# Kernel tuning notes

Hardware: AMD Instinct MI355X
Metric: run time of the kernel (lower is better)

The kernel has to match this reference:

```python
import jax, jax.numpy as jnp
import numpy as np

H = 16  # n_heads (init kwarg)


def pos_enc(length, dim):
    # torch PositionalEncoding: pe[:,0::2]=sin, pe[:,1::2]=cos
    pos = jnp.arange(length, dtype=jnp.float32)[:, None]
    div = jnp.exp(jnp.arange(0, dim, 2, dtype=jnp.float32) * (-np.log(10000.0) / dim))
    ang = pos * div  # [L, dim/2]
    return jnp.stack([jnp.sin(ang), jnp.cos(ang)], axis=-1).reshape(length, dim)


def torch_ln(x, a, b, eps=1e-6):
    # custom LayerNorm: a*(x-mean)/(std+eps)+b with unbiased std (torch default)
    mean = x.mean(-1, keepdims=True)
    n = x.shape[-1]
    var = ((x - mean) ** 2).sum(-1, keepdims=True) / (n - 1)
    return a * (x - mean) / (jnp.sqrt(var) + eps) + b


def setup_inputs() -> dict:
    key = jax.random.key(0)
    ks = jax.random.split(key, 16)
    B, Lq, Lk, qd, kd, hid, mid = 8, 512, 1024, 768, 768, 1024, 4096
    s = 0.02  # weight init scale
    w = lambda k, shape: jax.random.normal(k, shape, jnp.float32) * s
    return dict(
        q=jax.random.normal(ks[0], (B, Lq, qd), jnp.float32),
        k=jax.random.normal(ks[1], (B, Lk, kd), jnp.float32),
        Wq=w(ks[2], (qd, hid)), bq=jnp.zeros(hid, jnp.float32),
        Wk=w(ks[3], (kd, hid)), bk=jnp.zeros(hid, jnp.float32),
        Wv=w(ks[4], (kd, hid)), bv=jnp.zeros(hid, jnp.float32),
        Wv0=w(ks[5], (kd, hid)), bv0=jnp.zeros(hid, jnp.float32),
        Wq0=w(ks[6], (qd, hid)), bq0=jnp.zeros(hid, jnp.float32),
        nq_a=jnp.ones(hid, jnp.float32), nq_b=jnp.zeros(hid, jnp.float32),
        nx_a=jnp.ones(hid, jnp.float32), nx_b=jnp.zeros(hid, jnp.float32),
        W1=w(ks[7], (hid, mid)), b1=jnp.zeros(mid, jnp.float32),
        W2=w(ks[8], (mid, hid)), b2=jnp.zeros(hid, jnp.float32),
        ns_a=jnp.ones(hid, jnp.float32), ns_b=jnp.zeros(hid, jnp.float32),
    )


def reference(q, k, Wq, bq, Wk, bk, Wv, bv, Wv0, bv0, Wq0, bq0,
              nq_a, nq_b, nx_a, nx_b, W1, b1, W2, b2, ns_a, ns_b):
    # FocalAtt(mode='CA').forward(q, k, PE='qk', SF=True, outmode='atted_bilinear')
    B, Lq, qd = q.shape
    Lk, kd = k.shape[1], k.shape[2]
    hid = Wq.shape[1]
    dh = hid // H
    q0 = q
    qp = q + pos_enc(Lq, qd)  # PosEnc_q (dropout=0)
    kp = k + pos_enc(Lk, kd)  # PosEnc_k
    # AttM: manual multi-head scores
    qh = (qp @ Wq + bq).reshape(B, Lq, H, dh).transpose(0, 2, 1, 3)  # bhqd
    kh = (kp @ Wk + bk).reshape(B, Lk, H, dh).transpose(0, 2, 1, 3)  # bhkd
    scores = jnp.einsum('bhqd,bhkd->bhqk', qh, kh) / jnp.sqrt(jnp.float32(dh))
    att = jax.nn.softmax(scores, axis=-1)  # SF=True
    q0p = q0 @ Wq0 + bq0  # [B, Lq, hid]
    # 'atted' branch
    v1 = (kp @ Wv + bv).reshape(B, Lk, H, dh).transpose(0, 2, 1, 3)
    atted = jnp.einsum('bhqk,bhkd->bhqd', att, v1)
    atted = atted.transpose(0, 2, 1, 3).reshape(B, Lq, hid)
    atted = torch_ln(q0p + atted, nq_a, nq_b)
    # 'bilinear' branch: einsum('bhvk,bhvq,bhqk->bhk')
    q0h = q0p.reshape(B, Lq, H, dh).transpose(0, 2, 1, 3)  # bhvd, v=Lq
    v0 = (kp @ Wv0 + bv0).reshape(B, Lk, H, dh).transpose(0, 2, 1, 3)  # bhqd, q=Lk
    x = jnp.einsum('bhvd,bhvq,bhqd->bhd', q0h, att, v0).reshape(B, hid)
    x = torch_ln(x, nx_a, nx_b)
    # attention output: relu over scores, mean over heads
    att_out = jax.nn.relu(scores).sum(axis=1) / jnp.float32(H)  # [B, Lq, Lk]
    # SorCA: FFN + residual + LayerNorm
    ff = jax.nn.relu(atted @ W1 + b1) @ W2 + b2
    qq = torch_ln(atted + ff, ns_a, ns_b)
    # FocalAtt returns (feature, q, k, attention, attidx_q, attidx_k); drop Nones
    return (x, qq, kp, att_out)
```

## Files before the change

### kernel.cpp

```cpp
#include <hip/hip_runtime.h>


typedef unsigned short bfr;
using short8 = __attribute__((ext_vector_type(8))) short;
using f32x4  = __attribute__((ext_vector_type(4))) float;

__device__ __forceinline__ float b2f(bfr s) {
  return __uint_as_float(((unsigned int)s) << 16);
}
__device__ __forceinline__ bfr f2b(float f) {
  unsigned int u = __float_as_uint(f);
  u += 0x7fffu + ((u >> 16) & 1u);
  return (bfr)(u >> 16);
}

struct __align__(8) us4 { bfr x, y, z, w; };

__device__ __forceinline__ float4 load4f(const float* p) { return *(const float4*)p; }
__device__ __forceinline__ float4 load4f(const bfr* p) {
  us4 u = *(const us4*)p;
  return make_float4(b2f(u.x), b2f(u.y), b2f(u.z), b2f(u.w));
}
__device__ __forceinline__ void store4(float* p, float a, float b, float c, float d) {
  *(float4*)p = make_float4(a, b, c, d);
}
__device__ __forceinline__ void store4(bfr* p, float a, float b, float c, float d) {
  us4 v; v.x = f2b(a); v.y = f2b(b); v.z = f2b(c); v.w = f2b(d);
  *(us4*)p = v;
}

__device__ __forceinline__ void gll16(const bfr* g, bfr* l) {
  __builtin_amdgcn_global_load_lds(
      (const __attribute__((address_space(1))) unsigned int*)g,
      (__attribute__((address_space(3))) unsigned int*)l, 16, 0, 0);
}

__device__ __forceinline__ float pe_val(int l, int d) {
  float ang = (float)l * expf((float)(d & ~1) * (-9.210340371976184f / 768.0f));
  return (d & 1) ? cosf(ang) : sinf(ang);
}

__global__ __launch_bounds__(256) void posenc_k(const float* __restrict__ in,
                                                float* __restrict__ outf,
                                                bfr* __restrict__ outb, int total) {
  int idx = blockIdx.x * 256 + threadIdx.x;
  if (idx >= total) return;
  float v = in[idx] + pe_val((idx / 768) % 1024, idx % 768);
  outf[idx] = v;
  outb[idx] = f2b(v);
}

__global__ __launch_bounds__(256) void posenc_q_all(const float* __restrict__ in,
                                                    bfr* __restrict__ out,
                                                    bfr* __restrict__ outraw,
                                                    int total) {
  int idx = blockIdx.x * 256 + threadIdx.x;
  if (idx >= total) return;
  float v = in[idx];
  out[idx] = f2b(v + pe_val((idx / 768) % 512, idx % 768));
  outraw[idx] = f2b(v);
}

__global__ __launch_bounds__(256) void transpose_w(const float* __restrict__ src,
                                                   bfr* __restrict__ dst,
                                                   int rows, int cols, int ld,
                                                   int mode) {
  __shared__ float t[32][33];
  const int bc = blockIdx.x * 32, br = blockIdx.y * 32;
  const int tx = threadIdx.x & 31, ty = threadIdx.x >> 5;
#pragma unroll
  for (int i = 0; i < 4; i++)
    t[ty + i * 8][tx] = src[(size_t)(br + ty + i * 8) * ld + bc + tx];
  __syncthreads();
#pragma unroll
  for (int i = 0; i < 4; i++) {
    int c = bc + ty + i * 8;
    int r = (mode == 0) ? c : ((c >> 6) * 128 + (c & 63) + (mode == 2 ? 64 : 0));
    dst[(size_t)r * rows + br + tx] = f2b(t[tx][ty + i * 8]);
  }
}

template <typename TC>
__device__ __forceinline__ void mgemm_body(const bfr* __restrict__ A,
                                           const bfr* __restrict__ BT,
                                           const float* __restrict__ bias,
                                           TC* __restrict__ C,
                                           int K, int ldc, int relu, int accum,
                                           int m0, int n0,
                                           bfr* __restrict__ As,
                                           bfr* __restrict__ Bs) {
  const int tid = threadIdx.x;
  const int lane = tid & 63, w = tid >> 6;
  const int wm = (w & 1) * 64, wn = (w >> 1) * 64;
  const int grow = w * 32 + (lane >> 3);
  const int gkc = (lane & 7) * 8;
  const int fr = lane & 15, fc = (lane >> 4) * 8;
  const int NT = K >> 6;
  f32x4 acc[4][4];
#pragma unroll
  for (int i = 0; i < 4; i++)
#pragma unroll
    for (int j = 0; j < 4; j++) acc[i][j] = (f32x4){0.f, 0.f, 0.f, 0.f};

  auto issue = [&](int t, int buf) {
    const int k0 = t << 6;
    const bfr* Ag = A + (size_t)(m0 + grow) * K + k0 + gkc;
    const bfr* Bg = BT + (size_t)(n0 + grow) * K + k0 + gkc;
#pragma unroll
    for (int i = 0; i < 4; i++)
      gll16(Ag + (size_t)(i * 8) * K, As + buf * 8192 + (w * 32 + i * 8) * 64);
#pragma unroll
    for (int i = 0; i < 4; i++)
      gll16(Bg + (size_t)(i * 8) * K, Bs + buf * 8192 + (w * 32 + i * 8) * 64);
  };

  issue(0, 0);
  __syncthreads();
  int cur = 0;
  for (int t = 0; t < NT; ++t) {
    const bool more = (t + 1 < NT);
    if (more) issue(t + 1, cur ^ 1);
    __builtin_amdgcn_s_setprio(1);
#pragma unroll
    for (int ks = 0; ks < 2; ks++) {
      short8 af[4], bf4[4];
#pragma unroll
      for (int i = 0; i < 4; i++)
        af[i] = *(const short8*)(As + cur * 8192 + (wm + i * 16 + fr) * 64 + ks * 32 + fc);
#pragma unroll
      for (int i = 0; i < 4; i++)
        bf4[i] = *(const short8*)(Bs + cur * 8192 + (wn + i * 16 + fr) * 64 + ks * 32 + fc);
#pragma unroll
      for (int i = 0; i < 4; i++)
#pragma unroll
        for (int j = 0; j < 4; j++)
          acc[i][j] = __builtin_amdgcn_mfma_f32_16x16x32_bf16(af[i], bf4[j], acc[i][j], 0, 0, 0);
    }
    __builtin_amdgcn_s_setprio(0);
    if (more) {
      __syncthreads();
      cur ^= 1;
    }
  }
  const int col0 = n0 + wn + fr;
  const int row0 = m0 + wm + (lane >> 4) * 4;
  float bsv[4];
#pragma unroll
  for (int j = 0; j < 4; j++) bsv[j] = bias ? bias[col0 + j * 16] : 0.f;
#pragma unroll
  for (int i = 0; i < 4; i++) {
#pragma unroll
    for (int j = 0; j < 4; j++) {
      const int col = col0 + j * 16;
#pragma unroll
      for (int r = 0; r < 4; r++) {
        const int row = row0 + i * 16 + r;
        float v = acc[i][j][r] + bsv[j];
        if (relu) v = fmaxf(v, 0.f);
        size_t idx = (size_t)row * ldc + col;
        if constexpr (sizeof(TC) == 2) {
          C[idx] = f2b(v);
        } else {
          if (accum) C[idx] += v; else C[idx] = v;
        }
      }
    }
  }
}

template <typename TC>
__device__ __forceinline__ void mgemm_body64(const bfr* __restrict__ A,
                                             const bfr* __restrict__ BT,
                                             const float* __restrict__ bias,
                                             TC* __restrict__ C,
                                             int K, int ldc, int relu, int accum,
                                             int m0, int n0,
                                             bfr* __restrict__ As,
                                             bfr* __restrict__ Bs) {
  const int tid = threadIdx.x;
  const int lane = tid & 63, w = tid >> 6;
  const int wm = (w & 1) * 64, wn = (w >> 1) * 32;
  const int grow = lane >> 3, gkc = (lane & 7) * 8;
  const int fr = lane & 15, fc = (lane >> 4) * 8;
  const int NT = K >> 6;
  f32x4 acc[4][2];
#pragma unroll
  for (int i = 0; i < 4; i++)
#pragma unroll
    for (int j = 0; j < 2; j++) acc[i][j] = (f32x4){0.f, 0.f, 0.f, 0.f};

  auto issue = [&](int t, int buf) {
    const int k0 = t << 6;
    const bfr* Ag = A + (size_t)(m0 + w * 32 + grow) * K + k0 + gkc;
#pragma unroll
    for (int i = 0; i < 4; i++)
      gll16(Ag + (size_t)(i * 8) * K, As + buf * 8192 + (w * 32 + i * 8) * 64);
    const bfr* Bg = BT + (size_t)(n0 + w * 16 + grow) * K + k0 + gkc;
#pragma unroll
    for (int i = 0; i < 2; i++)
      gll16(Bg + (size_t)(i * 8) * K, Bs + buf * 4096 + (w * 16 + i * 8) * 64);
  };

  issue(0, 0);
  __syncthreads();
  int cur = 0;
  for (int t = 0; t < NT; ++t) {
    const bool more = (t + 1 < NT);
    if (more) issue(t + 1, cur ^ 1);
    __builtin_amdgcn_s_setprio(1);
#pragma unroll
    for (int ks = 0; ks < 2; ks++) {
      short8 af[4], bf4[2];
#pragma unroll
      for (int i = 0; i < 4; i++)
        af[i] = *(const short8*)(As + cur * 8192 + (wm + i * 16 + fr) * 64 + ks * 32 + fc);
#pragma unroll
      for (int j = 0; j < 2; j++)
        bf4[j] = *(const short8*)(Bs + cur * 4096 + (wn + j * 16 + fr) * 64 + ks * 32 + fc);
#pragma unroll
      for (int i = 0; i < 4; i++)
#pragma unroll
        for (int j = 0; j < 2; j++)
          acc[i][j] = __builtin_amdgcn_mfma_f32_16x16x32_bf16(af[i], bf4[j], acc[i][j], 0, 0, 0);
    }
    __builtin_amdgcn_s_setprio(0);
    if (more) {
      __syncthreads();
      cur ^= 1;
    }
  }
  const int col0 = n0 + wn + fr;
  const int row0 = m0 + wm + (lane >> 4) * 4;
  float bsv[2];
#pragma unroll
  for (int j = 0; j < 2; j++) bsv[j] = bias ? bias[col0 + j * 16] : 0.f;
#pragma unroll
  for (int i = 0; i < 4; i++) {
#pragma unroll
    for (int j = 0; j < 2; j++) {
      const int col = col0 + j * 16;
#pragma unroll
      for (int r = 0; r < 4; r++) {
        const int row = row0 + i * 16 + r;
        float v = acc[i][j][r] + bsv[j];
        if (relu) v = fmaxf(v, 0.f);
        size_t idx = (size_t)row * ldc + col;
        if constexpr (sizeof(TC) == 2) {
          C[idx] = f2b(v);
        } else {
          if (accum) C[idx] += v; else C[idx] = v;
        }
      }
    }
  }
}

template <typename TC>
__global__ __launch_bounds__(256) void mgemm(const bfr* __restrict__ A,
                                             const bfr* __restrict__ BT,
                                             const float* __restrict__ bias,
                                             TC* __restrict__ C,
                                             int K, int ldc, int relu, int accum) {
  __shared__ bfr As[2][8192];
  __shared__ bfr Bs[2][8192];
  const int nwg = gridDim.x * gridDim.y;
  const int bid = blockIdx.y * gridDim.x + blockIdx.x;
  const int q8 = nwg >> 3, r8 = nwg & 7;
  const int xcd = bid & 7, off = bid >> 3;
  const int swz = (xcd < r8 ? xcd * (q8 + 1) : r8 * (q8 + 1) + (xcd - r8) * q8) + off;
  const int n0 = (swz % gridDim.x) * 128, m0 = (swz / gridDim.x) * 128;
  mgemm_body<TC>(A, BT, bias, C, K, ldc, relu, accum, m0, n0,
                 &As[0][0], &Bs[0][0]);
}

template <typename TC>
__global__ __launch_bounds__(256) void mgemm64(const bfr* __restrict__ A,
                                               const bfr* __restrict__ BT,
                                               const float* __restrict__ bias,
                                               TC* __restrict__ C,
                                               int K, int ldc, int relu, int accum) {
  __shared__ bfr As[2][8192];
  __shared__ bfr Bs[2][4096];
  const int nwg = gridDim.x * gridDim.y;
  const int bid = blockIdx.y * gridDim.x + blockIdx.x;
  const int q8 = nwg >> 3, r8 = nwg & 7;
  const int xcd = bid & 7, off = bid >> 3;
  const int swz = (xcd < r8 ? xcd * (q8 + 1) : r8 * (q8 + 1) + (xcd - r8) * q8) + off;
  const int n0 = (swz % gridDim.x) * 64, m0 = (swz / gridDim.x) * 128;
  mgemm_body64<TC>(A, BT, bias, C, K, ldc, relu, accum, m0, n0,
                   &As[0][0], &Bs[0][0]);
}

__global__ __launch_bounds__(256) void kv_gemm2(const bfr* __restrict__ kp0,
                                                const bfr* __restrict__ kp1,
                                                const bfr* __restrict__ WkT,
                                                const float* __restrict__ bk,
                                                bfr* __restrict__ kh0,
                                                bfr* __restrict__ kh1,
                                                const bfr* __restrict__ WTvv,
                                                bfr* __restrict__ vT0,
                                                bfr* __restrict__ vT1) {
  __shared__ bfr As[2][8192];
  __shared__ bfr Bs[2][4096];
  const int swz = (blockIdx.x & 7) * 96 + (blockIdx.x >> 3);
  if (swz < 128) {
    mgemm_body64<bfr>(kp0, WkT, bk, kh0, 768, 1024, 0, 0,
                      (swz >> 4) * 128, (swz & 15) * 64, &As[0][0], &Bs[0][0]);
  } else if (swz < 256) {
    const int s = swz - 128;
    mgemm_body64<bfr>(kp1, WkT, bk, kh1, 768, 1024, 0, 0,
                      (s >> 4) * 128, (s & 15) * 64, &As[0][0], &Bs[0][0]);
  } else if (swz < 512) {
    const int s = swz - 256;
    mgemm_body64<bfr>(WTvv, kp0, nullptr, vT0, 768, 1024, 0, 0,
                      (s >> 4) * 128, (s & 15) * 64, &As[0][0], &Bs[0][0]);
  } else {
    const int s = swz - 512;
    mgemm_body64<bfr>(WTvv, kp1, nullptr, vT1, 768, 1024, 0, 0,
                      (s >> 4) * 128, (s & 15) * 64, &As[0][0], &Bs[0][0]);
  }
}

__global__ __launch_bounds__(256) void proj_gemm(const bfr* __restrict__ q16,
                                                 const bfr* __restrict__ Wq0T,
                                                 const float* __restrict__ bq0,
                                                 bfr* __restrict__ q0p,
                                                 const bfr* __restrict__ qp_all,
                                                 const bfr* __restrict__ WqT,
                                                 const float* __restrict__ bq,
                                                 bfr* __restrict__ qh) {
  __shared__ bfr As[2][8192];
  __shared__ bfr Bs[2][8192];
  const int swz = (blockIdx.x & 7) * 64 + (blockIdx.x >> 3);
  if (swz < 256) {
    mgemm_body<bfr>(q16, Wq0T, bq0, q0p, 768, 1024, 0, 0,
                    (swz >> 3) * 128, (swz & 7) * 128, &As[0][0], &Bs[0][0]);
  } else {
    const int s = swz - 256;
    mgemm_body<bfr>(qp_all, WqT, bq, qh, 768, 1024, 0, 0,
                    (s >> 3) * 128, (s & 7) * 128, &As[0][0], &Bs[0][0]);
  }
}

__global__ __launch_bounds__(256) void score_mfma(const bfr* __restrict__ qh,
                                                  const bfr* __restrict__ kh,
                                                  bfr* __restrict__ sc) {
  __shared__ __align__(16) bfr Qs[128][72];
  __shared__ __align__(16) bfr Ks[128][72];
  const int h = blockIdx.z, q0 = blockIdx.y * 128, k0 = blockIdx.x * 128;
  const int tid = threadIdx.x, lane = tid & 63;
  const int wm = ((tid >> 6) & 1) * 64, wn = (tid >> 7) * 64;
  const int fr = lane & 15, fc = (lane >> 4) * 8;
  {
    const int r = tid >> 1, c = (tid & 1) * 32;
    const bfr* qsrc = qh + (size_t)(q0 + r) * 1024 + h * 64 + c;
    const bfr* ksrc = kh + (size_t)(k0 + r) * 1024 + h * 64 + c;
#pragma unroll
    for (int i = 0; i < 4; i++) {
      *(short8*)&Qs[r][c + i * 8] = *(const short8*)(qsrc + i * 8);
      *(short8*)&Ks[r][c + i * 8] = *(const short8*)(ksrc + i * 8);
    }
  }
  __syncthreads();
  f32x4 acc[4][4];
#pragma unroll
  for (int i = 0; i < 4; i++)
#pragma unroll
    for (int j = 0; j < 4; j++) acc[i][j] = (f32x4){0.f, 0.f, 0.f, 0.f};
  __builtin_amdgcn_s_setprio(1);
#pragma unroll
  for (int ks = 0; ks < 2; ks++) {
    short8 af[4], bf[4];
#pragma unroll
    for (int t = 0; t < 4; t++) af[t] = *(const short8*)&Qs[wm + t * 16 + fr][ks * 32 + fc];
#pragma unroll
    for (int t = 0; t < 4; t++) bf[t] = *(const short8*)&Ks[wn + t * 16 + fr][ks * 32 + fc];
#pragma unroll
    for (int i = 0; i < 4; i++)
#pragma unroll
      for (int j = 0; j < 4; j++)
        acc[i][j] = __builtin_amdgcn_mfma_f32_16x16x32_bf16(af[i], bf[j], acc[i][j], 0, 0, 0);
  }
  __builtin_amdgcn_s_setprio(0);
  const int col0 = k0 + wn + fr;
  const int row0 = q0 + wm + (lane >> 4) * 4;
#pragma unroll
  for (int i = 0; i < 4; i++)
#pragma unroll
    for (int j = 0; j < 4; j++)
#pragma unroll
      for (int r = 0; r < 4; r++)
        sc[((size_t)h * 512 + row0 + i * 16 + r) * 1024 + col0 + j * 16] =
            f2b(acc[i][j][r] * 0.125f);
}

__global__ __launch_bounds__(256) void smax_ao(bfr* __restrict__ sc,
                                               float* __restrict__ ao) {
  __shared__ float part[4][1024];
  const int q = blockIdx.x;
  const int tid = threadIdx.x, lane = tid & 63, w = tid >> 6;
  float aos[16];
#pragma unroll
  for (int i = 0; i < 16; i++) aos[i] = 0.f;
#pragma unroll
  for (int i = 0; i < 4; i++) {
    const int h = w * 4 + i;
    bfr* row = sc + ((size_t)h * 512 + q) * 1024 + lane * 16;
    us4 raw[4];
    float v[16];
#pragma unroll
    for (int j = 0; j < 4; j++) raw[j] = ((const us4*)row)[j];
#pragma unroll
    for (int j = 0; j < 4; j++) {
      v[j * 4 + 0] = b2f(raw[j].x); v[j * 4 + 1] = b2f(raw[j].y);
      v[j * 4 + 2] = b2f(raw[j].z); v[j * 4 + 3] = b2f(raw[j].w);
    }
    float m = v[0];
#pragma unroll
    for (int j = 1; j < 16; j++) m = fmaxf(m, v[j]);
#pragma unroll
    for (int j = 0; j < 16; j++) aos[j] += fmaxf(v[j], 0.f);
    for (int o = 32; o; o >>= 1) m = fmaxf(m, __shfl_xor(m, o, 64));
    float s = 0.f;
#pragma unroll
    for (int j = 0; j < 16; j++) { v[j] = expf(v[j] - m); s += v[j]; }
    for (int o = 32; o; o >>= 1) s += __shfl_xor(s, o, 64);
    const float inv = 1.0f / s;
#pragma unroll
    for (int j = 0; j < 4; j++) {
      raw[j].x = f2b(v[j * 4 + 0] * inv); raw[j].y = f2b(v[j * 4 + 1] * inv);
      raw[j].z = f2b(v[j * 4 + 2] * inv); raw[j].w = f2b(v[j * 4 + 3] * inv);
      ((us4*)row)[j] = raw[j];
    }
  }
#pragma unroll
  for (int j = 0; j < 4; j++)
    *(float4*)&part[w][lane * 16 + j * 4] =
        make_float4(aos[j * 4], aos[j * 4 + 1], aos[j * 4 + 2], aos[j * 4 + 3]);
  __syncthreads();
  const int k4 = tid * 4;
  float4 a0 = *(const float4*)&part[0][k4];
  float4 a1 = *(const float4*)&part[1][k4];
  float4 a2 = *(const float4*)&part[2][k4];
  float4 a3 = *(const float4*)&part[3][k4];
  store4(ao + (size_t)q * 1024 + k4,
         (a0.x + a1.x + a2.x + a3.x) * 0.0625f, (a0.y + a1.y + a2.y + a3.y) * 0.0625f,
         (a0.z + a1.z + a2.z + a3.z) * 0.0625f, (a0.w + a1.w + a2.w + a3.w) * 0.0625f);
}

__global__ __launch_bounds__(256) void attv2(const bfr* __restrict__ att,
                                             const bfr* __restrict__ vT,
                                             const float* __restrict__ bv,
                                             const float* __restrict__ bv0,
                                             bfr* __restrict__ atp,
                                             bfr* __restrict__ u) {
  __shared__ bfr As[2][32 * 64];
  __shared__ bfr Bs[2][128 * 64];
  const int h = blockIdx.y, q0 = blockIdx.x * 32;
  const int tid = threadIdx.x, lane = tid & 63, w = tid >> 6;
  const int fr = lane & 15, fc = (lane >> 4) * 8;
  const int wm = (w & 1) * 16, wn = (w >> 1) * 64;
  const bfr* attb = att + ((size_t)h * 512 + q0) * 1024;
  const bfr* vb = vT + (size_t)h * 128 * 1024;
  const int grow = lane >> 3, gkc = (lane & 7) * 8;
  f32x4 acc[4];
#pragma unroll
  for (int t = 0; t < 4; t++) acc[t] = (f32x4){0.f, 0.f, 0.f, 0.f};

  auto issue = [&](int t, int buf) {
    const int k0 = t << 6;
    gll16(attb + (size_t)(w * 8 + grow) * 1024 + k0 + gkc, &As[buf][(w * 8) * 64]);
#pragma unroll
    for (int i = 0; i < 4; i++)
      gll16(vb + (size_t)(w * 32 + i * 8 + grow) * 1024 + k0 + gkc,
            &Bs[buf][(w * 32 + i * 8) * 64]);
  };

  issue(0, 0);
  __syncthreads();
  int cur = 0;
  for (int t = 0; t < 16; ++t) {
    const bool more = (t + 1 < 16);
    if (more) issue(t + 1, cur ^ 1);
    __builtin_amdgcn_s_setprio(1);
#pragma unroll
    for (int ks = 0; ks < 2; ks++) {
      short8 af = *(const short8*)&As[cur][(wm + fr) * 64 + ks * 32 + fc];
#pragma unroll
      for (int j = 0; j < 4; j++) {
        short8 bf = *(const short8*)&Bs[cur][(wn + j * 16 + fr) * 64 + ks * 32 + fc];
        acc[j] = __builtin_amdgcn_mfma_f32_16x16x32_bf16(af, bf, acc[j], 0, 0, 0);
      }
    }
    __builtin_amdgcn_s_setprio(0);
    if (more) {
      __syncthreads();
      cur ^= 1;
    }
  }
  const int row0 = q0 + wm + (lane >> 4) * 4;
  bfr* o = (wn == 0) ? atp : u;
  const float* bias = (wn == 0) ? bv : bv0;
#pragma unroll
  for (int t = 0; t < 4; t++) {
    const int cm = t * 16 + fr;
    const float bb = bias[h * 64 + cm];
#pragma unroll
    for (int r = 0; r < 4; r++)
      o[(size_t)(row0 + r) * 1024 + h * 64 + cm] = f2b(acc[t][r] + bb);
  }
}

__global__ __launch_bounds__(256) void xpre_kernel(const bfr* __restrict__ q0p,
                                                   const bfr* __restrict__ u,
                                                   float* __restrict__ xpre) {
  const int c = blockIdx.x * 256 + threadIdx.x;
  const int r0 = blockIdx.y * 64;
  const bfr* qp = q0p + (size_t)r0 * 1024 + c;
  const bfr* up = u + (size_t)r0 * 1024 + c;
  float s = 0.f;
#pragma unroll 8
  for (int r = 0; r < 64; r++)
    s = fmaf(b2f(qp[(size_t)r * 1024]), b2f(up[(size_t)r * 1024]), s);
  atomicAdd(&xpre[c], s);
}

template <typename TX, typename TY, typename OT>
__global__ __launch_bounds__(256) void ln_kernel(const TX* __restrict__ X,
                                                 const TY* __restrict__ Y,
                                                 const float* __restrict__ ga,
                                                 const float* __restrict__ be,
                                                 OT* __restrict__ out) {
  __shared__ float sm[4];
  const size_t row = blockIdx.x;
  const int tid = threadIdx.x;
  float4 v = load4f(X + row * 1024 + tid * 4);
  if (Y) {
    float4 w = load4f(Y + row * 1024 + tid * 4);
    v.x += w.x; v.y += w.y; v.z += w.z; v.w += w.w;
  }
  float s = v.x + v.y + v.z + v.w;
  for (int o = 32; o; o >>= 1) s += __shfl_down(s, o, 64);
  if ((tid & 63) == 0) sm[tid >> 6] = s;
  __syncthreads();
  s = sm[0] + sm[1] + sm[2] + sm[3];
  float mean = s * (1.0f / 1024.0f);
  float d0 = v.x - mean, d1 = v.y - mean, d2 = v.z - mean, d3 = v.w - mean;
  float q = d0 * d0 + d1 * d1 + d2 * d2 + d3 * d3;
  __syncthreads();
  for (int o = 32; o; o >>= 1) q += __shfl_down(q, o, 64);
  if ((tid & 63) == 0) sm[tid >> 6] = q;
  __syncthreads();
  q = sm[0] + sm[1] + sm[2] + sm[3];
  float rs = 1.0f / (sqrtf(q * (1.0f / 1023.0f)) + 1e-6f);
  float4 g = *(const float4*)(ga + tid * 4);
  float4 bb = *(const float4*)(be + tid * 4);
  store4(out + row * 1024 + tid * 4,
         g.x * d0 * rs + bb.x, g.y * d1 * rs + bb.y,
         g.z * d2 * rs + bb.z, g.w * d3 * rs + bb.w);
}

extern "C" void kernel_launch(void* const* d_in, const int* in_sizes, int n_in,
                              void* d_out, int out_size, void* d_ws, size_t ws_size,
                              hipStream_t stream) {
  (void)in_sizes; (void)n_in; (void)out_size; (void)ws_size;
  const float* q   = (const float*)d_in[0];
  const float* k   = (const float*)d_in[1];
  const float* Wq  = (const float*)d_in[2];
  const float* bq  = (const float*)d_in[3];
  const float* Wk  = (const float*)d_in[4];
  const float* bk  = (const float*)d_in[5];
  const float* Wv  = (const float*)d_in[6];
  const float* bv  = (const float*)d_in[7];
  const float* Wv0 = (const float*)d_in[8];
  const float* bv0 = (const float*)d_in[9];
  const float* Wq0 = (const float*)d_in[10];
  const float* bq0 = (const float*)d_in[11];
  const float* nqa = (const float*)d_in[12];
  const float* nqb = (const float*)d_in[13];
  const float* nxa = (const float*)d_in[14];
  const float* nxb = (const float*)d_in[15];
  const float* W1  = (const float*)d_in[16];
  const float* b1  = (const float*)d_in[17];
  const float* W2  = (const float*)d_in[18];
  const float* b2  = (const float*)d_in[19];
  const float* nsa = (const float*)d_in[20];
  const float* nsb = (const float*)d_in[21];

  float* out = (float*)d_out;
  float* x_out  = out;
  float* qq_out = out + 8192;
  float* kp_out = out + 4202496;
  float* ao_out = out + 10493952;
  bfr* kp16 = (bfr*)qq_out;
  bfr* vT1  = kp16 + 6291456;

  char* base = (char*)d_ws;
  bfr* q0p   = (bfr*)(base + 0);
  bfr* qh    = (bfr*)(base + 8388608);
  bfr* atl   = (bfr*)(base + 16777216);
  bfr* WqT   = (bfr*)(base + 25165824);
  bfr* Wq0T  = (bfr*)(base + 26738688);
  bfr* WTkv  = (bfr*)(base + 28311552);
  float* xpre = (float*)(base + 33030144);
  char* S = base + 33062912;
  bfr* sc    = (bfr*)(S + 0);
  bfr* kh0   = (bfr*)(S + 16777216);
  bfr* kh1   = (bfr*)(S + 18874368);
  bfr* vT0   = (bfr*)(S + 20971520);
  bfr* atp0  = (bfr*)(S + 16777216);
  bfr* ub0   = (bfr*)(S + 17825792);
  bfr* atp1  = (bfr*)(S + 18874368);
  bfr* ub1   = (bfr*)(S + 19922944);
  bfr* qp_all = (bfr*)(S + 0);
  bfr* q16    = (bfr*)(S + 6291456);
  bfr* W1Tn  = (bfr*)(S + 0);
  bfr* W2Tn  = (bfr*)(S + 4194304);
  bfr* ff1n  = (bfr*)(S + 8388608);
  float* ff2a = (float*)(base + 0);

  posenc_k<<<24576, 256, 0, stream>>>(k, kp_out, kp16, 6291456);
  posenc_q_all<<<12288, 256, 0, stream>>>(q, qp_all, q16, 3145728);
  transpose_w<<<dim3(32, 24), 256, 0, stream>>>(Wq, WqT, 768, 1024, 1024, 0);
  transpose_w<<<dim3(32, 24), 256, 0, stream>>>(Wq0, Wq0T, 768, 1024, 1024, 0);
  transpose_w<<<dim3(32, 24), 256, 0, stream>>>(Wk, WTkv, 768, 1024, 1024, 0);
  transpose_w<<<dim3(32, 24), 256, 0, stream>>>(Wv, WTkv + 786432, 768, 1024, 1024, 1);
  transpose_w<<<dim3(32, 24), 256, 0, stream>>>(Wv0, WTkv + 786432, 768, 1024, 1024, 2);

  proj_gemm<<<512, 256, 0, stream>>>(q16, Wq0T, bq0, q0p, qp_all, WqT, bq, qh);
  hipMemsetAsync(xpre, 0, 32768, stream);

  for (int p = 0; p < 4; p++) {
    const int b0 = 2 * p, b1 = 2 * p + 1;
    kv_gemm2<<<768, 256, 0, stream>>>(kp16 + (size_t)b0 * 786432,
                                      kp16 + (size_t)b1 * 786432,
                                      WTkv, bk, kh0, kh1,
                                      WTkv + 786432, vT0, vT1);
    for (int j = 0; j < 2; j++) {
      const int b = b0 + j;
      bfr* kh = j ? kh1 : kh0;
      bfr* vT = j ? vT1 : vT0;
      bfr* atpb = j ? atp1 : atp0;
      bfr* ub = j ? ub1 : ub0;
      score_mfma<<<dim3(8, 4, 16), 256, 0, stream>>>(qh + (size_t)b * 524288, kh, sc);
      smax_ao<<<512, 256, 0, stream>>>(sc, ao_out + (size_t)b * 524288);
      attv2<<<dim3(16, 16), 256, 0, stream>>>(sc, vT, bv, bv0, atpb, ub);
      xpre_kernel<<<dim3(4, 8), 256, 0, stream>>>(q0p + (size_t)b * 524288, ub,
                                                  xpre + b * 1024);
      ln_kernel<bfr, bfr, bfr><<<512, 256, 0, stream>>>(
          q0p + (size_t)b * 524288, atpb, nqa, nqb, atl + (size_t)b * 524288);
    }
  }

  ln_kernel<float, float, float><<<8, 256, 0, stream>>>(xpre, (const float*)nullptr,
                                                        nxa, nxb, x_out);

  for (int nc = 0; nc < 2; nc++) {
    transpose_w<<<dim3(64, 32), 256, 0, stream>>>(W1 + nc * 2048, W1Tn,
                                                  1024, 2048, 4096, 0);
    transpose_w<<<dim3(32, 64), 256, 0, stream>>>(W2 + (size_t)nc * 2048 * 1024, W2Tn,
                                                  2048, 1024, 1024, 0);
    mgemm<bfr><<<dim3(16, 32), 256, 0, stream>>>(
        atl, W1Tn, b1 + nc * 2048, ff1n, 1024, 2048, 1, 0);
    mgemm64<float><<<dim3(16, 32), 256, 0, stream>>>(
        ff1n, W2Tn, nc == 0 ? b2 : nullptr, ff2a, 2048, 1024, 0, nc);
  }
  ln_kernel<bfr, float, float><<<4096, 256, 0, stream>>>(atl, ff2a, nsa, nsb, qq_out);
}
```

Measured before the change: 801.1 us.

## Triple-buffer GEMM LDS pipeline with XOR swizzle and unify on 128x64 tiles

The GEMM bodies move from double to triple buffering in LDS. Loads are issued two tiles ahead, and explicit vmcnt waits replace __syncthreads. LDS rows are XOR-swizzled to avoid bank conflicts on the MFMA fragment reads. The 128x128 mgemm path is removed, and the projection and FFN1 GEMMs now use the 128x64 tile kernel with twice the grid. This aims to hide global load latency and raise occupancy, but it uses more LDS per block and relies on correct hand-counted vmcnt values.

```diff
diff --git a/kernel.cpp b/kernel.cpp
--- a/kernel.cpp
+++ b/kernel.cpp
@@ -33,6 +33,10 @@
   __builtin_amdgcn_global_load_lds(
       (const __attribute__((address_space(1))) unsigned int*)g,
       (__attribute__((address_space(3))) unsigned int*)l, 16, 0, 0);
+}
+
+__device__ __forceinline__ int swz_off(int row, int chunk) {
+  return row * 64 + ((chunk ^ (row & 7)) * 8);
 }
 
 __device__ __forceinline__ float pe_val(int l, int d) {
@@ -77,94 +81,6 @@
     int c = bc + ty + i * 8;
     int r = (mode == 0) ? c : ((c >> 6) * 128 + (c & 63) + (mode == 2 ? 64 : 0));
     dst[(size_t)r * rows + br + tx] = f2b(t[tx][ty + i * 8]);
-  }
-}
-
-template <typename TC>
-__device__ __forceinline__ void mgemm_body(const bfr* __restrict__ A,
-                                           const bfr* __restrict__ BT,
-                                           const float* __restrict__ bias,
-                                           TC* __restrict__ C,
-                                           int K, int ldc, int relu, int accum,
-                                           int m0, int n0,
-                                           bfr* __restrict__ As,
-                                           bfr* __restrict__ Bs) {
-  const int tid = threadIdx.x;
-  const int lane = tid & 63, w = tid >> 6;
-  const int wm = (w & 1) * 64, wn = (w >> 1) * 64;
-  const int grow = w * 32 + (lane >> 3);
-  const int gkc = (lane & 7) * 8;
-  const int fr = lane & 15, fc = (lane >> 4) * 8;
-  const int NT = K >> 6;
-  f32x4 acc[4][4];
-#pragma unroll
-  for (int i = 0; i < 4; i++)
-#pragma unroll
-    for (int j = 0; j < 4; j++) acc[i][j] = (f32x4){0.f, 0.f, 0.f, 0.f};
-
-  auto issue = [&](int t, int buf) {
-    const int k0 = t << 6;
-    const bfr* Ag = A + (size_t)(m0 + grow) * K + k0 + gkc;
-    const bfr* Bg = BT + (size_t)(n0 + grow) * K + k0 + gkc;
-#pragma unroll
-    for (int i = 0; i < 4; i++)
-      gll16(Ag + (size_t)(i * 8) * K, As + buf * 8192 + (w * 32 + i * 8) * 64);
-#pragma unroll
-    for (int i = 0; i < 4; i++)
-      gll16(Bg + (size_t)(i * 8) * K, Bs + buf * 8192 + (w * 32 + i * 8) * 64);
-  };
-
-  issue(0, 0);
-  __syncthreads();
-  int cur = 0;
-  for (int t = 0; t < NT; ++t) {
-    const bool more = (t + 1 < NT);
-    if (more) issue(t + 1, cur ^ 1);
-    __builtin_amdgcn_s_setprio(1);
-#pragma unroll
-    for (int ks = 0; ks < 2; ks++) {
-      short8 af[4], bf4[4];
-#pragma unroll
-      for (int i = 0; i < 4; i++)
-        af[i] = *(const short8*)(As + cur * 8192 + (wm + i * 16 + fr) * 64 + ks * 32 + fc);
-#pragma unroll
-      for (int i = 0; i < 4; i++)
-        bf4[i] = *(const short8*)(Bs + cur * 8192 + (wn + i * 16 + fr) * 64 + ks * 32 + fc);
-#pragma unroll
-      for (int i = 0; i < 4; i++)
-#pragma unroll
-        for (int j = 0; j < 4; j++)
-          acc[i][j] = __builtin_amdgcn_mfma_f32_16x16x32_bf16(af[i], bf4[j], acc[i][j], 0, 0, 0);
-    }
-    __builtin_amdgcn_s_setprio(0);
-    if (more) {
-      __syncthreads();
-      cur ^= 1;
-    }
-  }
-  const int col0 = n0 + wn + fr;
-  const int row0 = m0 + wm + (lane >> 4) * 4;
-  float bsv[4];
-#pragma unroll
-  for (int j = 0; j < 4; j++) bsv[j] = bias ? bias[col0 + j * 16] : 0.f;
-#pragma unroll
-  for (int i = 0; i < 4; i++) {
-#pragma unroll
-    for (int j = 0; j < 4; j++) {
-      const int col = col0 + j * 16;
-#pragma unroll
-      for (int r = 0; r < 4; r++) {
-        const int row = row0 + i * 16 + r;
-        float v = acc[i][j][r] + bsv[j];
-        if (relu) v = fmaxf(v, 0.f);
-        size_t idx = (size_t)row * ldc + col;
-        if constexpr (sizeof(TC) == 2) {
-          C[idx] = f2b(v);
-        } else {
-          if (accum) C[idx] += v; else C[idx] = v;
-        }
-      }
-    }
   }
 }
 
@@ -180,8 +96,9 @@
   const int tid = threadIdx.x;
   const int lane = tid & 63, w = tid >> 6;
   const int wm = (w & 1) * 64, wn = (w >> 1) * 32;
-  const int grow = lane >> 3, gkc = (lane & 7) * 8;
-  const int fr = lane & 15, fc = (lane >> 4) * 8;
+  const int grow = lane >> 3;
+  const int gkc = ((lane & 7) ^ (lane >> 3)) * 8;
+  const int fr = lane & 15, fcg = lane >> 4;
   const int NT = K >> 6;
   f32x4 acc[4][2];
 #pragma unroll
@@ -202,21 +119,26 @@
   };
 
   issue(0, 0);
-  __syncthreads();
-  int cur = 0;
+  issue(1, 1);
+  asm volatile("s_waitcnt vmcnt(6)" ::: "memory");
+  __builtin_amdgcn_s_barrier();
+  __builtin_amdgcn_sched_barrier(0);
+  int cur = 0, ib = 2;
   for (int t = 0; t < NT; ++t) {
-    const bool more = (t + 1 < NT);
-    if (more) issue(t + 1, cur ^ 1);
+    if (t + 2 < NT) {
+      issue(t + 2, ib);
+      ib = (ib == 2) ? 0 : ib + 1;
+    }
     __builtin_amdgcn_s_setprio(1);
 #pragma unroll
     for (int ks = 0; ks < 2; ks++) {
       short8 af[4], bf4[2];
 #pragma unroll
       for (int i = 0; i < 4; i++)
-        af[i] = *(const short8*)(As + cur * 8192 + (wm + i * 16 + fr) * 64 + ks * 32 + fc);
+        af[i] = *(const short8*)(As + cur * 8192 + swz_off(wm + i * 16 + fr, ks * 4 + fcg));
 #pragma unroll
       for (int j = 0; j < 2; j++)
-        bf4[j] = *(const short8*)(Bs + cur * 4096 + (wn + j * 16 + fr) * 64 + ks * 32 + fc);
+        bf4[j] = *(const short8*)(Bs + cur * 4096 + swz_off(wn + j * 16 + fr, ks * 4 + fcg));
 #pragma unroll
       for (int i = 0; i < 4; i++)
 #pragma unroll
@@ -224,9 +146,14 @@
           acc[i][j] = __builtin_amdgcn_mfma_f32_16x16x32_bf16(af[i], bf4[j], acc[i][j], 0, 0, 0);
     }
     __builtin_amdgcn_s_setprio(0);
-    if (more) {
-      __syncthreads();
-      cur ^= 1;
+    if (t + 1 < NT) {
+      if (t + 2 < NT)
+        asm volatile("s_waitcnt vmcnt(6)" ::: "memory");
+      else
+        asm volatile("s_waitcnt vmcnt(0)" ::: "memory");
+      __builtin_amdgcn_s_barrier();
+      __builtin_amdgcn_sched_barrier(0);
+      cur = (cur == 2) ? 0 : cur + 1;
     }
   }
   const int col0 = n0 + wn + fr;
@@ -256,31 +183,13 @@
 }
 
 template <typename TC>
-__global__ __launch_bounds__(256) void mgemm(const bfr* __restrict__ A,
-                                             const bfr* __restrict__ BT,
-                                             const float* __restrict__ bias,
-                                             TC* __restrict__ C,
-                                             int K, int ldc, int relu, int accum) {
-  __shared__ bfr As[2][8192];
-  __shared__ bfr Bs[2][8192];
-  const int nwg = gridDim.x * gridDim.y;
-  const int bid = blockIdx.y * gridDim.x + blockIdx.x;
-  const int q8 = nwg >> 3, r8 = nwg & 7;
-  const int xcd = bid & 7, off = bid >> 3;
-  const int swz = (xcd < r8 ? xcd * (q8 + 1) : r8 * (q8 + 1) + (xcd - r8) * q8) + off;
-  const int n0 = (swz % gridDim.x) * 128, m0 = (swz / gridDim.x) * 128;
-  mgemm_body<TC>(A, BT, bias, C, K, ldc, relu, accum, m0, n0,
-                 &As[0][0], &Bs[0][0]);
-}
-
-template <typename TC>
 __global__ __launch_bounds__(256) void mgemm64(const bfr* __restrict__ A,
                                                const bfr* __restrict__ BT,
                                                const float* __restrict__ bias,
                                                TC* __restrict__ C,
                                                int K, int ldc, int relu, int accum) {
-  __shared__ bfr As[2][8192];
-  __shared__ bfr Bs[2][4096];
+  __shared__ bfr As[3][8192];
+  __shared__ bfr Bs[3][4096];
   const int nwg = gridDim.x * gridDim.y;
   const int bid = blockIdx.y * gridDim.x + blockIdx.x;
   const int q8 = nwg >> 3, r8 = nwg & 7;
@@ -300,8 +209,8 @@
                                                 const bfr* __restrict__ WTvv,
                                                 bfr* __restrict__ vT0,
                                                 bfr* __restrict__ vT1) {
-  __shared__ bfr As[2][8192];
-  __shared__ bfr Bs[2][4096];
+  __shared__ bfr As[3][8192];
+  __shared__ bfr Bs[3][4096];
   const int swz = (blockIdx.x & 7) * 96 + (blockIdx.x >> 3);
   if (swz < 128) {
     mgemm_body64<bfr>(kp0, WkT, bk, kh0, 768, 1024, 0, 0,
@@ -329,16 +238,16 @@
                                                  const bfr* __restrict__ WqT,
                                                  const float* __restrict__ bq,
                                                  bfr* __restrict__ qh) {
-  __shared__ bfr As[2][8192];
-  __shared__ bfr Bs[2][8192];
-  const int swz = (blockIdx.x & 7) * 64 + (blockIdx.x >> 3);
-  if (swz < 256) {
-    mgemm_body<bfr>(q16, Wq0T, bq0, q0p, 768, 1024, 0, 0,
-                    (swz >> 3) * 128, (swz & 7) * 128, &As[0][0], &Bs[0][0]);
+  __shared__ bfr As[3][8192];
+  __shared__ bfr Bs[3][4096];
+  const int swz = (blockIdx.x & 7) * 128 + (blockIdx.x >> 3);
+  if (swz < 512) {
+    mgemm_body64<bfr>(q16, Wq0T, bq0, q0p, 768, 1024, 0, 0,
+                      (swz >> 4) * 128, (swz & 15) * 64, &As[0][0], &Bs[0][0]);
   } else {
-    const int s = swz - 256;
-    mgemm_body<bfr>(qp_all, WqT, bq, qh, 768, 1024, 0, 0,
-                    (s >> 3) * 128, (s & 7) * 128, &As[0][0], &Bs[0][0]);
+    const int s = swz - 512;
+    mgemm_body64<bfr>(qp_all, WqT, bq, qh, 768, 1024, 0, 0,
+                      (s >> 4) * 128, (s & 15) * 64, &As[0][0], &Bs[0][0]);
   }
 }
 
@@ -454,15 +363,16 @@
                                              const float* __restrict__ bv0,
                                              bfr* __restrict__ atp,
                                              bfr* __restrict__ u) {
-  __shared__ bfr As[2][32 * 64];
-  __shared__ bfr Bs[2][128 * 64];
+  __shared__ bfr As[3][32 * 64];
+  __shared__ bfr Bs[3][128 * 64];
   const int h = blockIdx.y, q0 = blockIdx.x * 32;
   const int tid = threadIdx.x, lane = tid & 63, w = tid >> 6;
-  const int fr = lane & 15, fc = (lane >> 4) * 8;
+  const int fr = lane & 15, fcg = lane >> 4;
   const int wm = (w & 1) * 16, wn = (w >> 1) * 64;
   const bfr* attb = att + ((size_t)h * 512 + q0) * 1024;
   const bfr* vb = vT + (size_t)h * 128 * 1024;
-  const int grow = lane >> 3, gkc = (lane & 7) * 8;
+  const int grow = lane >> 3;
+  const int gkc = ((lane & 7) ^ (lane >> 3)) * 8;
   f32x4 acc[4];
 #pragma unroll
   for (int t = 0; t < 4; t++) acc[t] = (f32x4){0.f, 0.f, 0.f, 0.f};
@@ -477,25 +387,35 @@
   };
 
   issue(0, 0);
-  __syncthreads();
-  int cur = 0;
+  issue(1, 1);
+  asm volatile("s_waitcnt vmcnt(5)" ::: "memory");
+  __builtin_amdgcn_s_barrier();
+  __builtin_amdgcn_sched_barrier(0);
+  int cur = 0, ib = 2;
   for (int t = 0; t < 16; ++t) {
-    const bool more = (t + 1 < 16);
-    if (more) issue(t + 1, cur ^ 1);
+    if (t + 2 < 16) {
+      issue(t + 2, ib);
+      ib = (ib == 2) ? 0 : ib + 1;
+    }
     __builtin_amdgcn_s_setprio(1);
 #pragma unroll
     for (int ks = 0; ks < 2; ks++) {
-      short8 af = *(const short8*)&As[cur][(wm + fr) * 64 + ks * 32 + fc];
+      short8 af = *(const short8*)&As[cur][swz_off(wm + fr, ks * 4 + fcg)];
 #pragma unroll
       for (int j = 0; j < 4; j++) {
-        short8 bf = *(const short8*)&Bs[cur][(wn + j * 16 + fr) * 64 + ks * 32 + fc];
+        short8 bf = *(const short8*)&Bs[cur][swz_off(wn + j * 16 + fr, ks * 4 + fcg)];
         acc[j] = __builtin_amdgcn_mfma_f32_16x16x32_bf16(af, bf, acc[j], 0, 0, 0);
       }
     }
     __builtin_amdgcn_s_setprio(0);
-    if (more) {
-      __syncthreads();
-      cur ^= 1;
+    if (t + 1 < 16) {
+      if (t + 2 < 16)
+        asm volatile("s_waitcnt vmcnt(5)" ::: "memory");
+      else
+        asm volatile("s_waitcnt vmcnt(0)" ::: "memory");
+      __builtin_amdgcn_s_barrier();
+      __builtin_amdgcn_sched_barrier(0);
+      cur = (cur == 2) ? 0 : cur + 1;
     }
   }
   const int row0 = q0 + wm + (lane >> 4) * 4;
@@ -627,7 +547,7 @@
   transpose_w<<<dim3(32, 24), 256, 0, stream>>>(Wv, WTkv + 786432, 768, 1024, 1024, 1);
   transpose_w<<<dim3(32, 24), 256, 0, stream>>>(Wv0, WTkv + 786432, 768, 1024, 1024, 2);
 
-  proj_gemm<<<512, 256, 0, stream>>>(q16, Wq0T, bq0, q0p, qp_all, WqT, bq, qh);
+  proj_gemm<<<1024, 256, 0, stream>>>(q16, Wq0T, bq0, q0p, qp_all, WqT, bq, qh);
   hipMemsetAsync(xpre, 0, 32768, stream);
 
   for (int p = 0; p < 4; p++) {
@@ -660,7 +580,7 @@
                                                   1024, 2048, 4096, 0);
     transpose_w<<<dim3(32, 64), 256, 0, stream>>>(W2 + (size_t)nc * 2048 * 1024, W2Tn,
                                                   2048, 1024, 1024, 0);
-    mgemm<bfr><<<dim3(16, 32), 256, 0, stream>>>(
+    mgemm64<bfr><<<dim3(32, 32), 256, 0, stream>>>(
         atl, W1Tn, b1 + nc * 2048, ff1n, 1024, 2048, 1, 0);
     mgemm64<float><<<dim3(16, 32), 256, 0, stream>>>(
         ff1n, W2Tn, nc == 0 ? b2 : nullptr, ff2a, 2048, 1024, 0, nc);
```

Result: faster. 780.0 us (-2.6%).
